# Kernel optimization log

Hardware: AMD Instinct MI355X
Metric: run time of the kernel (lower is better)

Reference implementation:

```python
import jax, jax.numpy as jnp
import numpy as np

S, B, DIM = 1024, 4, 768
N_EXPERTS = 8
# hidden_dim = 256 * ceil(int(2*4*dim/3)/256) = 2048 for dim=768
HID = 2048


def setup_inputs() -> dict:
    key = jax.random.key(0)
    ks = jax.random.split(key, 6)
    scale = 0.02
    return {
        "hidden_states": jax.random.normal(ks[0], (S, B, DIM), dtype=jnp.float32),
        "router_w": jax.random.normal(ks[1], (DIM, N_EXPERTS), dtype=jnp.float32) * scale,
        "router_b": jnp.zeros((N_EXPERTS,), dtype=jnp.float32),
        "w1": jax.random.normal(ks[2], (N_EXPERTS, DIM, HID), dtype=jnp.float32) * scale,
        "w2": jax.random.normal(ks[3], (N_EXPERTS, DIM, HID), dtype=jnp.float32) * scale,
        "w3": jax.random.normal(ks[4], (N_EXPERTS, HID, DIM), dtype=jnp.float32) * scale,
    }


def reference(hidden_states, router_w, router_b, w1, w2, w3):
    s, b, h = hidden_states.shape
    # top-1 router
    route = jax.nn.softmax(hidden_states @ router_w + router_b, axis=2)  # [s,b,E]
    max_prob = jnp.max(route, axis=2).reshape(-1, 1)   # [T,1]
    max_ind = jnp.argmax(route, axis=2).reshape(-1)    # [T]
    x = hidden_states.reshape(-1, h)                   # [T,d]

    out = jnp.zeros_like(x)
    # fixed small loop over experts; masked dispatch (tokens not routed to e
    # are zeroed so they contribute nothing)
    for e in range(N_EXPERTS):
        mask = (max_ind == e)[:, None]                 # [T,1]
        xe = jnp.where(mask, x, 0.0)
        oe = (jax.nn.silu(xe @ w1[e]) * (xe @ w2[e])) @ w3[e]
        out = out + jnp.where(mask, oe, 0.0)

    # original stores expert outputs in a bf16 buffer before the prob combine
    out = out.astype(jnp.bfloat16) * max_prob          # bf16 * f32 -> f32
    return out.reshape(s, b, h)
```

## Files before the change

### kernel.cpp

```cpp
#include <hip/hip_runtime.h>


#define T_TOK 4096
#define DIM   768
#define HID   2048
#define NE    8
#define ECAP  1024

#define KB1 (DIM / 32)
#define NB1 (HID / 16)
#define KB2 (HID / 32)
#define NB2 (DIM / 16)
#define MBC (ECAP / 16)

typedef _Float16 f16x8 __attribute__((ext_vector_type(8)));
typedef _Float16 f16x4 __attribute__((ext_vector_type(4)));
typedef float    f32x4 __attribute__((ext_vector_type(4)));

__device__ __forceinline__ float bf16_rne(float v) {
    unsigned u = __float_as_uint(v);
    unsigned r = (u + 0x7fffu + ((u >> 16) & 1u)) & 0xffff0000u;
    return __uint_as_float(r);
}

__global__ void moe_init_kernel(int* __restrict__ counts) {
    if (threadIdx.x < NE) counts[threadIdx.x] = 0;
}

__global__ __launch_bounds__(256) void moe_convert_kernel(
    const float* __restrict__ w1, const float* __restrict__ w2,
    const float* __restrict__ w3, _Float16* __restrict__ w1s,
    _Float16* __restrict__ w2s, _Float16* __restrict__ w3s)
{
    const int z = blockIdx.z, e = z & 7, mat = z >> 3;
    const float* src; _Float16* dst; int K, N;
    if (mat == 0)      { src = w1 + (size_t)e * DIM * HID; dst = w1s + (size_t)e * NB1 * KB1 * 512; K = DIM; N = HID; }
    else if (mat == 1) { src = w2 + (size_t)e * DIM * HID; dst = w2s + (size_t)e * NB1 * KB1 * 512; K = DIM; N = HID; }
    else               { src = w3 + (size_t)e * HID * DIM; dst = w3s + (size_t)e * NB2 * KB2 * 512; K = HID; N = DIM; }
    const int ngrp = blockIdx.x, kb = blockIdx.y;
    if (ngrp * 128 >= N || kb * 32 >= K) return;
    const int KBc = K >> 5;

    __shared__ _Float16 Lt[128 * 40];
    const int t  = threadIdx.x;
    const int n4 = (t & 31) * 4;
    const int k4 = (t >> 5) * 4;
    const float* p = src + (size_t)(kb * 32 + k4) * N + ngrp * 128 + n4;
    float4 v[4];
#pragma unroll
    for (int j = 0; j < 4; ++j) v[j] = *(const float4*)(p + (size_t)j * N);
#pragma unroll
    for (int i = 0; i < 4; ++i) {
        f16x4 q;
#pragma unroll
        for (int j = 0; j < 4; ++j) q[j] = (_Float16)(((const float*)&v[j])[i]);
        *(f16x4*)&Lt[(n4 + i) * 40 + k4] = q;
    }
    __syncthreads();
    const int w = t >> 6, l = t & 63;
#pragma unroll
    for (int c = 0; c < 2; ++c) {
        const int nbl = w * 2 + c;
        f16x8 fr = *(const f16x8*)&Lt[(nbl * 16 + (l & 15)) * 40 + (l >> 4) * 8];
        const int nb = ngrp * 8 + nbl;
        *(f16x8*)(dst + ((size_t)nb * KBc + kb) * 512 + l * 8) = fr;
    }
}

__global__ __launch_bounds__(256) void moe_router_kernel(
    const float* __restrict__ X, const float* __restrict__ rw,
    const float* __restrict__ rb, float* __restrict__ probs,
    int* __restrict__ counts, int* __restrict__ lists)
{
    const int t    = blockIdx.x * 4 + (threadIdx.x >> 6);
    const int lane = threadIdx.x & 63;
    const float* x = X + (size_t)t * DIM;

    float xv[12];
#pragma unroll
    for (int j = 0; j < 12; ++j) xv[j] = x[lane + j * 64];

    double lg[NE];
#pragma unroll
    for (int e = 0; e < NE; ++e) {
        double s = 0.0;
#pragma unroll
        for (int j = 0; j < 12; ++j)
            s += (double)xv[j] * (double)rw[(lane + j * 64) * NE + e];
#pragma unroll
        for (int off = 32; off >= 1; off >>= 1) s += __shfl_xor(s, off, 64);
        lg[e] = s + (double)rb[e];
    }

    if (lane == 0) {
        double m = lg[0]; int mi = 0;
#pragma unroll
        for (int e = 1; e < NE; ++e)
            if (lg[e] > m) { m = lg[e]; mi = e; }
        float sum = 0.f;
#pragma unroll
        for (int e = 0; e < NE; ++e) sum += expf((float)(lg[e] - m));
        probs[t] = 1.0f / sum;
        int pos = atomicAdd(&counts[mi], 1);
        lists[mi * T_TOK + pos] = t;
    }
}

__global__ __launch_bounds__(256) void moe_gather_kernel(
    const float* __restrict__ X, const int* __restrict__ lists,
    const int* __restrict__ counts, _Float16* __restrict__ Ag)
{
    const int e = blockIdx.z;
    int cnt = counts[e]; if (cnt > ECAP) cnt = ECAP;
    const int mgrp = blockIdx.y;
    if (mgrp * 64 >= ((cnt + 63) & ~63)) return;
    const int t = threadIdx.x, w = t >> 6, l = t & 63;
    const int mb = mgrp * 4 + w;
    const int m  = mb * 16 + (l & 15);
    const bool valid = (m < cnt);
    const int tok = valid ? lists[e * T_TOK + m] : 0;
    const float* xr = X + (size_t)tok * DIM + (l >> 4) * 8;
#pragma unroll
    for (int i = 0; i < 4; ++i) {
        const int kb = blockIdx.x * 4 + i;
        float4 a = make_float4(0.f, 0.f, 0.f, 0.f), b = a;
        if (valid) {
            a = *(const float4*)(xr + kb * 32);
            b = *(const float4*)(xr + kb * 32 + 4);
        }
        f16x8 h;
        h[0] = (_Float16)a.x; h[1] = (_Float16)a.y; h[2] = (_Float16)a.z; h[3] = (_Float16)a.w;
        h[4] = (_Float16)b.x; h[5] = (_Float16)b.y; h[6] = (_Float16)b.z; h[7] = (_Float16)b.w;
        *(f16x8*)(Ag + ((size_t)(e * MBC + mb) * KB1 + kb) * 512 + l * 8) = h;
    }
}

__global__ __launch_bounds__(256) void moe_gemm1_kernel(
    const _Float16* __restrict__ Ag, const _Float16* __restrict__ w1s,
    const _Float16* __restrict__ w2s, const int* __restrict__ counts,
    _Float16* __restrict__ Hs)
{
    const int e = blockIdx.z;
    int cnt = counts[e]; if (cnt > ECAP) cnt = ECAP;
    const int by = blockIdx.y, bx = blockIdx.x;
    if (by * 64 >= cnt) return;
    const int t = threadIdx.x, w = t >> 6, l = t & 63;

    const _Float16* Ab  = Ag  + ((size_t)(e * MBC + by * 4) * KB1) * 512 + l * 8;
    const int nb0 = bx * 8 + w * 2;
    const _Float16* B1b = w1s + ((size_t)(e * NB1 + nb0) * KB1) * 512 + l * 8;
    const _Float16* B2b = w2s + ((size_t)(e * NB1 + nb0) * KB1) * 512 + l * 8;

    f32x4 acc1[4][2], acc2[4][2];
    const f32x4 zero = {0.f, 0.f, 0.f, 0.f};
#pragma unroll
    for (int i = 0; i < 4; ++i)
#pragma unroll
        for (int j = 0; j < 2; ++j) { acc1[i][j] = zero; acc2[i][j] = zero; }

#pragma unroll 2
    for (int kb = 0; kb < KB1; ++kb) {
        f16x8 a[4], b1[2], b2[2];
#pragma unroll
        for (int i = 0; i < 4; ++i)
            a[i] = *(const f16x8*)(Ab + (i * KB1 + kb) * 512);
#pragma unroll
        for (int j = 0; j < 2; ++j) {
            b1[j] = *(const f16x8*)(B1b + (j * KB1 + kb) * 512);
            b2[j] = *(const f16x8*)(B2b + (j * KB1 + kb) * 512);
        }
#pragma unroll
        for (int i = 0; i < 4; ++i)
#pragma unroll
            for (int j = 0; j < 2; ++j) {
                acc1[i][j] = __builtin_amdgcn_mfma_f32_16x16x32_f16(a[i], b1[j], acc1[i][j], 0, 0, 0);
                acc2[i][j] = __builtin_amdgcn_mfma_f32_16x16x32_f16(a[i], b2[j], acc2[i][j], 0, 0, 0);
            }
    }

    __shared__ _Float16 Ep[4][64 * 40];
    const int fq = l >> 4, fr = l & 15;
#pragma unroll
    for (int i = 0; i < 4; ++i)
#pragma unroll
        for (int j = 0; j < 2; ++j)
#pragma unroll
            for (int r = 0; r < 4; ++r) {
                const float h1 = acc1[i][j][r], h2 = acc2[i][j][r];
                const float s  = h1 / (1.f + __expf(-h1)) * h2;
                Ep[w][(i * 16 + fq * 4 + r) * 40 + j * 16 + fr] = (_Float16)s;
            }
    __syncthreads();
    const int kbH = bx * 4 + w;
#pragma unroll
    for (int i = 0; i < 4; ++i) {
        f16x8 v = *(const f16x8*)&Ep[w][(i * 16 + fr) * 40 + fq * 8];
        *(f16x8*)(Hs + ((size_t)(e * MBC + by * 4 + i) * KB2 + kbH) * 512 + l * 8) = v;
    }
}

__global__ __launch_bounds__(256) void moe_gemm2_kernel(
    const _Float16* __restrict__ Hs, const _Float16* __restrict__ w3s,
    const int* __restrict__ lists, const int* __restrict__ counts,
    const float* __restrict__ probs, float* __restrict__ out)
{
    const int e = blockIdx.z;
    int cnt = counts[e]; if (cnt > ECAP) cnt = ECAP;
    const int by = blockIdx.y, bx = blockIdx.x;
    const int m0 = by * 32;
    if (m0 >= cnt) return;
    const int t = threadIdx.x, w = t >> 6, l = t & 63;

    const _Float16* Ab = Hs  + ((size_t)(e * MBC + by * 2) * KB2) * 512 + l * 8;
    const int nb0 = bx * 8 + w * 2;
    const _Float16* Bb = w3s + ((size_t)(e * NB2 + nb0) * KB2) * 512 + l * 8;

    f32x4 acc[2][2];
    const f32x4 zero = {0.f, 0.f, 0.f, 0.f};
    acc[0][0] = zero; acc[0][1] = zero; acc[1][0] = zero; acc[1][1] = zero;

#pragma unroll 4
    for (int kb = 0; kb < KB2; ++kb) {
        f16x8 a[2], b[2];
#pragma unroll
        for (int i = 0; i < 2; ++i)
            a[i] = *(const f16x8*)(Ab + (i * KB2 + kb) * 512);
#pragma unroll
        for (int j = 0; j < 2; ++j)
            b[j] = *(const f16x8*)(Bb + (j * KB2 + kb) * 512);
#pragma unroll
        for (int i = 0; i < 2; ++i)
#pragma unroll
            for (int j = 0; j < 2; ++j)
                acc[i][j] = __builtin_amdgcn_mfma_f32_16x16x32_f16(a[i], b[j], acc[i][j], 0, 0, 0);
    }

    const int* list = lists + e * T_TOK;
    const int fq = l >> 4, fr = l & 15;
    const int c0 = bx * 128 + w * 32;
#pragma unroll
    for (int i = 0; i < 2; ++i)
#pragma unroll
        for (int r = 0; r < 4; ++r) {
            const int m = m0 + i * 16 + fq * 4 + r;
            if (m < cnt) {
                const int tok = list[m];
                const float pb = probs[tok];
                float* orow = out + (size_t)tok * DIM + c0 + fr;
                orow[0]  = bf16_rne(acc[i][0][r]) * pb;
                orow[16] = bf16_rne(acc[i][1][r]) * pb;
            }
        }
}

extern "C" void kernel_launch(void* const* d_in, const int* in_sizes, int n_in,
                              void* d_out, int out_size, void* d_ws, size_t ws_size,
                              hipStream_t stream) {
    const float* X  = (const float*)d_in[0];
    const float* rw = (const float*)d_in[1];
    const float* rb = (const float*)d_in[2];
    const float* w1 = (const float*)d_in[3];
    const float* w2 = (const float*)d_in[4];
    const float* w3 = (const float*)d_in[5];
    float* out = (float*)d_out;

    char* ws = (char*)d_ws;
    int*      counts = (int*)(ws + 0);
    int*      lists  = (int*)(ws + 256);
    float*    probs  = (float*)(ws + 131328);
    const size_t WSZ = 25165824;
    _Float16* w1s = (_Float16*)(ws + 147712);
    _Float16* w2s = (_Float16*)(ws + 147712 + WSZ);
    _Float16* w3s = (_Float16*)(ws + 147712 + 2 * WSZ);
    _Float16* Ag  = (_Float16*)(ws + 147712 + 3 * WSZ);
    _Float16* Hs  = (_Float16*)(ws + 147712 + 3 * WSZ + 12582912);

    hipLaunchKernelGGL(moe_init_kernel, dim3(1), dim3(64), 0, stream, counts);
    hipLaunchKernelGGL(moe_convert_kernel, dim3(16, 64, 24), dim3(256), 0, stream,
                       w1, w2, w3, w1s, w2s, w3s);
    hipLaunchKernelGGL(moe_router_kernel, dim3(T_TOK / 4), dim3(256), 0, stream,
                       X, rw, rb, probs, counts, lists);
    hipLaunchKernelGGL(moe_gather_kernel, dim3(6, 16, 8), dim3(256), 0, stream,
                       X, lists, counts, Ag);
    hipLaunchKernelGGL(moe_gemm1_kernel, dim3(16, 16, 8), dim3(256), 0, stream,
                       Ag, w1s, w2s, counts, Hs);
    hipLaunchKernelGGL(moe_gemm2_kernel, dim3(6, 32, 8), dim3(256), 0, stream,
                       Hs, w3s, lists, counts, probs, out);
}
```

Measured before the change: 349.2 us.

## Retile convert and expert GEMMs with register double-buffering and occupancy hints

The weight convert kernel now uses a flat grid of blocks, each moving a 64x128 fp32 tile through an fp32 LDS stage, so every thread issues more loads per block and the grid has no idle blocks. GEMM1 uses 128-row by 64-column block tiles with a 2x2 wave layout, and GEMM2 doubles each wave's M tile to 64 rows, raising per-block reuse of the weight fragments. Both GEMM main loops double-buffer fragment loads in registers to overlap global loads with MFMA, and launch bounds are set to cap register use. The cost is higher register pressure and fewer blocks per expert when token counts are low.

```diff
diff --git a/kernel.cpp b/kernel.cpp
--- a/kernel.cpp
+++ b/kernel.cpp
@@ -7,14 +7,13 @@
 #define NE    8
 #define ECAP  1024
 
-#define KB1 (DIM / 32)
-#define NB1 (HID / 16)
-#define KB2 (HID / 32)
-#define NB2 (DIM / 16)
-#define MBC (ECAP / 16)
+#define KB1 24
+#define NB1 128
+#define KB2 64
+#define NB2 48
+#define MBC 64
 
 typedef _Float16 f16x8 __attribute__((ext_vector_type(8)));
-typedef _Float16 f16x4 __attribute__((ext_vector_type(4)));
 typedef float    f32x4 __attribute__((ext_vector_type(4)));
 
 __device__ __forceinline__ float bf16_rne(float v) {
@@ -32,38 +31,50 @@
     const float* __restrict__ w3, _Float16* __restrict__ w1s,
     _Float16* __restrict__ w2s, _Float16* __restrict__ w3s)
 {
-    const int z = blockIdx.z, e = z & 7, mat = z >> 3;
-    const float* src; _Float16* dst; int K, N;
-    if (mat == 0)      { src = w1 + (size_t)e * DIM * HID; dst = w1s + (size_t)e * NB1 * KB1 * 512; K = DIM; N = HID; }
-    else if (mat == 1) { src = w2 + (size_t)e * DIM * HID; dst = w2s + (size_t)e * NB1 * KB1 * 512; K = DIM; N = HID; }
-    else               { src = w3 + (size_t)e * HID * DIM; dst = w3s + (size_t)e * NB2 * KB2 * 512; K = HID; N = DIM; }
-    const int ngrp = blockIdx.x, kb = blockIdx.y;
-    if (ngrp * 128 >= N || kb * 32 >= K) return;
-    const int KBc = K >> 5;
-
-    __shared__ _Float16 Lt[128 * 40];
+    const int bid = blockIdx.x;
+    const float* src; _Float16* dst; int N, KBc, ngrp, kgrp;
+    if (bid < 1536) {
+        const int e = bid / 192, tile = bid % 192;
+        src = w1 + (size_t)e * DIM * HID; dst = w1s + (size_t)e * NB1 * KB1 * 512;
+        N = HID; KBc = KB1; ngrp = tile & 15; kgrp = tile >> 4;
+    } else if (bid < 3072) {
+        const int r = bid - 1536, e = r / 192, tile = r % 192;
+        src = w2 + (size_t)e * DIM * HID; dst = w2s + (size_t)e * NB1 * KB1 * 512;
+        N = HID; KBc = KB1; ngrp = tile & 15; kgrp = tile >> 4;
+    } else {
+        const int r = bid - 3072, e = r / 192, tile = r % 192;
+        src = w3 + (size_t)e * HID * DIM; dst = w3s + (size_t)e * NB2 * KB2 * 512;
+        N = DIM; KBc = KB2; ngrp = tile % 6; kgrp = tile / 6;
+    }
+
+    __shared__ float Lt[64 * 130];
     const int t  = threadIdx.x;
-    const int n4 = (t & 31) * 4;
-    const int k4 = (t >> 5) * 4;
-    const float* p = src + (size_t)(kb * 32 + k4) * N + ngrp * 128 + n4;
-    float4 v[4];
-#pragma unroll
-    for (int j = 0; j < 4; ++j) v[j] = *(const float4*)(p + (size_t)j * N);
+    const int c4 = (t & 31) * 4;
+    const int r0 = (t >> 5) * 8;
+    const float* p = src + (size_t)(kgrp * 64 + r0) * N + ngrp * 128 + c4;
+    float4 v[8];
+#pragma unroll
+    for (int j = 0; j < 8; ++j) v[j] = *(const float4*)(p + (size_t)j * N);
+#pragma unroll
+    for (int j = 0; j < 8; ++j) {
+        float* row = &Lt[(r0 + j) * 130 + c4];
+        *(float2*)(row)     = make_float2(v[j].x, v[j].y);
+        *(float2*)(row + 2) = make_float2(v[j].z, v[j].w);
+    }
+    __syncthreads();
+
+    const int l = t & 63, w = t >> 6;
+    const int fr = l & 15, fq = l >> 4;
 #pragma unroll
     for (int i = 0; i < 4; ++i) {
-        f16x4 q;
-#pragma unroll
-        for (int j = 0; j < 4; ++j) q[j] = (_Float16)(((const float*)&v[j])[i]);
-        *(f16x4*)&Lt[(n4 + i) * 40 + k4] = q;
-    }
-    __syncthreads();
-    const int w = t >> 6, l = t & 63;
-#pragma unroll
-    for (int c = 0; c < 2; ++c) {
-        const int nbl = w * 2 + c;
-        f16x8 fr = *(const f16x8*)&Lt[(nbl * 16 + (l & 15)) * 40 + (l >> 4) * 8];
-        const int nb = ngrp * 8 + nbl;
-        *(f16x8*)(dst + ((size_t)nb * KBc + kb) * 512 + l * 8) = fr;
+        const int cell = w * 4 + i;
+        const int kbl = cell >> 3, nbl = cell & 7;
+        f16x8 h;
+#pragma unroll
+        for (int j = 0; j < 8; ++j)
+            h[j] = (_Float16)Lt[(kbl * 32 + fq * 8 + j) * 130 + nbl * 16 + fr];
+        const int nb = ngrp * 8 + nbl, kb = kgrp * 2 + kbl;
+        *(f16x8*)(dst + ((size_t)nb * KBc + kb) * 512 + l * 8) = h;
     }
 }
 
@@ -135,7 +146,7 @@
     }
 }
 
-__global__ __launch_bounds__(256) void moe_gemm1_kernel(
+__global__ __launch_bounds__(256, 3) void moe_gemm1_kernel(
     const _Float16* __restrict__ Ag, const _Float16* __restrict__ w1s,
     const _Float16* __restrict__ w2s, const int* __restrict__ counts,
     _Float16* __restrict__ Hs)
@@ -143,13 +154,14 @@
     const int e = blockIdx.z;
     int cnt = counts[e]; if (cnt > ECAP) cnt = ECAP;
     const int by = blockIdx.y, bx = blockIdx.x;
-    if (by * 64 >= cnt) return;
+    if (by * 128 >= cnt) return;
     const int t = threadIdx.x, w = t >> 6, l = t & 63;
-
-    const _Float16* Ab  = Ag  + ((size_t)(e * MBC + by * 4) * KB1) * 512 + l * 8;
-    const int nb0 = bx * 8 + w * 2;
-    const _Float16* B1b = w1s + ((size_t)(e * NB1 + nb0) * KB1) * 512 + l * 8;
-    const _Float16* B2b = w2s + ((size_t)(e * NB1 + nb0) * KB1) * 512 + l * 8;
+    const int wm = w & 1, wn = w >> 1;
+
+    const _Float16* Ab  = Ag + ((size_t)((e * MBC + by * 8 + wm * 4) * KB1)) * 512 + l * 8;
+    const int nb0 = e * NB1 + bx * 4 + wn * 2;
+    const _Float16* B1b = w1s + ((size_t)nb0 * KB1) * 512 + l * 8;
+    const _Float16* B2b = w2s + ((size_t)nb0 * KB1) * 512 + l * 8;
 
     f32x4 acc1[4][2], acc2[4][2];
     const f32x4 zero = {0.f, 0.f, 0.f, 0.f};
@@ -158,25 +170,39 @@
 #pragma unroll
         for (int j = 0; j < 2; ++j) { acc1[i][j] = zero; acc2[i][j] = zero; }
 
-#pragma unroll 2
-    for (int kb = 0; kb < KB1; ++kb) {
-        f16x8 a[4], b1[2], b2[2];
+    f16x8 a0[4], p0[2], q0[2], a1[4], p1[2], q1[2];
+
+    auto LD = [&](f16x8* a, f16x8* p, f16x8* q, int kb) {
 #pragma unroll
         for (int i = 0; i < 4; ++i)
-            a[i] = *(const f16x8*)(Ab + (i * KB1 + kb) * 512);
+            a[i] = *(const f16x8*)(Ab + ((size_t)(i * KB1 + kb)) * 512);
 #pragma unroll
         for (int j = 0; j < 2; ++j) {
-            b1[j] = *(const f16x8*)(B1b + (j * KB1 + kb) * 512);
-            b2[j] = *(const f16x8*)(B2b + (j * KB1 + kb) * 512);
+            p[j] = *(const f16x8*)(B1b + ((size_t)(j * KB1 + kb)) * 512);
+            q[j] = *(const f16x8*)(B2b + ((size_t)(j * KB1 + kb)) * 512);
         }
+    };
+    auto FM = [&](const f16x8* a, const f16x8* p, const f16x8* q) {
 #pragma unroll
         for (int i = 0; i < 4; ++i)
 #pragma unroll
             for (int j = 0; j < 2; ++j) {
-                acc1[i][j] = __builtin_amdgcn_mfma_f32_16x16x32_f16(a[i], b1[j], acc1[i][j], 0, 0, 0);
-                acc2[i][j] = __builtin_amdgcn_mfma_f32_16x16x32_f16(a[i], b2[j], acc2[i][j], 0, 0, 0);
+                acc1[i][j] = __builtin_amdgcn_mfma_f32_16x16x32_f16(a[i], p[j], acc1[i][j], 0, 0, 0);
+                acc2[i][j] = __builtin_amdgcn_mfma_f32_16x16x32_f16(a[i], q[j], acc2[i][j], 0, 0, 0);
             }
-    }
+    };
+
+    LD(a0, p0, q0, 0);
+    int kb = 0;
+    for (; kb + 2 < KB1; kb += 2) {
+        LD(a1, p1, q1, kb + 1);
+        FM(a0, p0, q0);
+        LD(a0, p0, q0, kb + 2);
+        FM(a1, p1, q1);
+    }
+    LD(a1, p1, q1, kb + 1);
+    FM(a0, p0, q0);
+    FM(a1, p1, q1);
 
     __shared__ _Float16 Ep[4][64 * 40];
     const int fq = l >> 4, fr = l & 15;
@@ -191,15 +217,15 @@
                 Ep[w][(i * 16 + fq * 4 + r) * 40 + j * 16 + fr] = (_Float16)s;
             }
     __syncthreads();
-    const int kbH = bx * 4 + w;
+    const int kbH = bx * 2 + wn;
 #pragma unroll
     for (int i = 0; i < 4; ++i) {
         f16x8 v = *(const f16x8*)&Ep[w][(i * 16 + fr) * 40 + fq * 8];
-        *(f16x8*)(Hs + ((size_t)(e * MBC + by * 4 + i) * KB2 + kbH) * 512 + l * 8) = v;
-    }
-}
-
-__global__ __launch_bounds__(256) void moe_gemm2_kernel(
+        *(f16x8*)(Hs + ((size_t)((e * MBC + by * 8 + wm * 4 + i) * KB2 + kbH)) * 512 + l * 8) = v;
+    }
+}
+
+__global__ __launch_bounds__(256, 4) void moe_gemm2_kernel(
     const _Float16* __restrict__ Hs, const _Float16* __restrict__ w3s,
     const int* __restrict__ lists, const int* __restrict__ counts,
     const float* __restrict__ probs, float* __restrict__ out)
@@ -207,42 +233,56 @@
     const int e = blockIdx.z;
     int cnt = counts[e]; if (cnt > ECAP) cnt = ECAP;
     const int by = blockIdx.y, bx = blockIdx.x;
-    const int m0 = by * 32;
-    if (m0 >= cnt) return;
+    if (by * 64 >= cnt) return;
     const int t = threadIdx.x, w = t >> 6, l = t & 63;
 
-    const _Float16* Ab = Hs  + ((size_t)(e * MBC + by * 2) * KB2) * 512 + l * 8;
-    const int nb0 = bx * 8 + w * 2;
-    const _Float16* Bb = w3s + ((size_t)(e * NB2 + nb0) * KB2) * 512 + l * 8;
-
-    f32x4 acc[2][2];
+    const _Float16* Ab = Hs + ((size_t)((e * MBC + by * 4) * KB2)) * 512 + l * 8;
+    const int nb0 = e * NB2 + bx * 8 + w * 2;
+    const _Float16* Bb = w3s + ((size_t)nb0 * KB2) * 512 + l * 8;
+
+    f32x4 acc[4][2];
     const f32x4 zero = {0.f, 0.f, 0.f, 0.f};
-    acc[0][0] = zero; acc[0][1] = zero; acc[1][0] = zero; acc[1][1] = zero;
-
-#pragma unroll 4
-    for (int kb = 0; kb < KB2; ++kb) {
-        f16x8 a[2], b[2];
-#pragma unroll
-        for (int i = 0; i < 2; ++i)
-            a[i] = *(const f16x8*)(Ab + (i * KB2 + kb) * 512);
+#pragma unroll
+    for (int i = 0; i < 4; ++i) { acc[i][0] = zero; acc[i][1] = zero; }
+
+    f16x8 a0[4], b0[2], a1[4], b1[2];
+
+    auto LD = [&](f16x8* a, f16x8* b, int kb) {
+#pragma unroll
+        for (int i = 0; i < 4; ++i)
+            a[i] = *(const f16x8*)(Ab + ((size_t)(i * KB2 + kb)) * 512);
 #pragma unroll
         for (int j = 0; j < 2; ++j)
-            b[j] = *(const f16x8*)(Bb + (j * KB2 + kb) * 512);
-#pragma unroll
-        for (int i = 0; i < 2; ++i)
+            b[j] = *(const f16x8*)(Bb + ((size_t)(j * KB2 + kb)) * 512);
+    };
+    auto FM = [&](const f16x8* a, const f16x8* b) {
+#pragma unroll
+        for (int i = 0; i < 4; ++i)
 #pragma unroll
             for (int j = 0; j < 2; ++j)
                 acc[i][j] = __builtin_amdgcn_mfma_f32_16x16x32_f16(a[i], b[j], acc[i][j], 0, 0, 0);
-    }
+    };
+
+    LD(a0, b0, 0);
+    int kb = 0;
+    for (; kb + 2 < KB2; kb += 2) {
+        LD(a1, b1, kb + 1);
+        FM(a0, b0);
+        LD(a0, b0, kb + 2);
+        FM(a1, b1);
+    }
+    LD(a1, b1, kb + 1);
+    FM(a0, b0);
+    FM(a1, b1);
 
     const int* list = lists + e * T_TOK;
     const int fq = l >> 4, fr = l & 15;
     const int c0 = bx * 128 + w * 32;
 #pragma unroll
-    for (int i = 0; i < 2; ++i)
+    for (int i = 0; i < 4; ++i)
 #pragma unroll
         for (int r = 0; r < 4; ++r) {
-            const int m = m0 + i * 16 + fq * 4 + r;
+            const int m = by * 64 + i * 16 + fq * 4 + r;
             if (m < cnt) {
                 const int tok = list[m];
                 const float pb = probs[tok];
@@ -276,14 +316,14 @@
     _Float16* Hs  = (_Float16*)(ws + 147712 + 3 * WSZ + 12582912);
 
     hipLaunchKernelGGL(moe_init_kernel, dim3(1), dim3(64), 0, stream, counts);
-    hipLaunchKernelGGL(moe_convert_kernel, dim3(16, 64, 24), dim3(256), 0, stream,
+    hipLaunchKernelGGL(moe_convert_kernel, dim3(4608), dim3(256), 0, stream,
                        w1, w2, w3, w1s, w2s, w3s);
     hipLaunchKernelGGL(moe_router_kernel, dim3(T_TOK / 4), dim3(256), 0, stream,
                        X, rw, rb, probs, counts, lists);
     hipLaunchKernelGGL(moe_gather_kernel, dim3(6, 16, 8), dim3(256), 0, stream,
                        X, lists, counts, Ag);
-    hipLaunchKernelGGL(moe_gemm1_kernel, dim3(16, 16, 8), dim3(256), 0, stream,
+    hipLaunchKernelGGL(moe_gemm1_kernel, dim3(32, 8, 8), dim3(256), 0, stream,
                        Ag, w1s, w2s, counts, Hs);
-    hipLaunchKernelGGL(moe_gemm2_kernel, dim3(6, 32, 8), dim3(256), 0, stream,
+    hipLaunchKernelGGL(moe_gemm2_kernel, dim3(6, 16, 8), dim3(256), 0, stream,
                        Hs, w3s, lists, counts, probs, out);
 }
```

Measured after the change: 340.5 us. 2.5% less time.
